# Kernel tuning notes

Hardware: AMD Instinct MI355X
Metric: run time of the kernel (lower is better)

The kernel has to match this reference:

```python
import jax, jax.numpy as jnp
import numpy as np

B, L, F, H = 4096, 32, 28, 512  # batch, max CDR length (=input_size), features, hidden


def setup_inputs() -> dict:
    key = jax.random.key(0)
    ks = jax.random.split(key, 8)
    return {
        "input": jax.random.normal(ks[0], (B, L, F), jnp.float32),
        "unpacked_masks": jnp.ones((B, L, 1), jnp.float32),
        "bias_mat": jnp.zeros((B, L, F), jnp.float32),
        "conv1_w": jax.random.normal(ks[1], (F, F, 3), jnp.float32) * 0.1,
        "conv1_b": jnp.zeros((F,), jnp.float32),
        "conv_w": jax.random.normal(ks[2], (1, L, 1), jnp.float32) * 0.1,
        "conv_b": jnp.zeros((1,), jnp.float32),
        "fc1_w": jax.random.normal(ks[3], (1, H), jnp.float32) * 0.05,
        "fc1_b": jnp.zeros((1,), jnp.float32),
        "W_ih": jax.random.normal(ks[4], (4 * H, L), jnp.float32) * 0.1,
        "W_hh": jax.random.normal(ks[5], (4 * H, H), jnp.float32) * 0.05,
        "b_ih": jnp.zeros((4 * H,), jnp.float32),
        "b_hh": jnp.zeros((4 * H,), jnp.float32),
        "conv2_w": jax.random.normal(ks[6], (1, H, 1), jnp.float32) * 0.05,
        "conv2_b": jnp.zeros((1,), jnp.float32),
    }


def reference(input, unpacked_masks, bias_mat, conv1_w, conv1_b, conv_w, conv_b,
              fc1_w, fc1_b, W_ih, W_hh, b_ih, b_hh, conv2_w, conv2_b):
    b, l, f = input.shape
    h_dim = W_hh.shape[1]
    # --- conv1 residual block (eval mode: dropouts are identity) ---
    x_t = jnp.transpose(input, (0, 2, 1))  # [B, F, L]
    y = jax.lax.conv_general_dilated(
        x_t, conv1_w, window_strides=(1,), padding=[(1, 1)],
        dimension_numbers=("NCH", "OIH", "NCH")) + conv1_b[None, :, None]
    x = jnp.transpose(y, (0, 2, 1)) * unpacked_masks  # [B, L, F]
    x = jax.nn.elu(x) + input
    # --- u_a = Conv1d(L,1,1) over the length axis: [B, 1, F] (kept as [B, F]) ---
    u_a = jnp.einsum("blf,l->bf", x, conv_w[0, :, 0]) + conv_b  # [B, F]
    x_transposed = jnp.transpose(x, (0, 2, 1))  # [B, F, L]

    h0 = jnp.zeros((l, h_dim), input.dtype)
    c0 = jnp.zeros((l, h_dim), input.dtype)

    def step(carry, inps):
        h, c = carry
        u_b, xT_b, bias_b = inps  # [F], [F, L], [L, F]
        w_a = h @ fc1_w.T + fc1_b  # [L, 1]
        scores = jax.nn.leaky_relu(u_b[None, :] + w_a, 0.01) + bias_b  # [L, F]
        attn = jax.nn.softmax(scores, axis=0)  # softmax over dim 1 of [B, L, F]
        ctx = attn @ xT_b  # [L, F] @ [F, L] -> [L, L]
        gates = ctx @ W_ih.T + b_ih + h @ W_hh.T + b_hh  # [L, 4H]
        i_g, f_g, g_g, o_g = jnp.split(gates, 4, axis=-1)
        c_new = jax.nn.sigmoid(f_g) * c + jax.nn.sigmoid(i_g) * jnp.tanh(g_g)
        h_new = jax.nn.sigmoid(o_g) * jnp.tanh(c_new)
        return (h_new, c_new), h_new

    # The original loops over the batch dim, carrying (h, c) across iterations.
    (_, _), all_hidden = jax.lax.scan(step, (h0, c0), (u_a, x_transposed, bias_mat))
    # all_hidden: [B, L, H]
    out = jnp.einsum("blh,h->bl", all_hidden, conv2_w[0, :, 0])[..., None] + conv2_b  # [B, L, 1]
    return out * unpacked_masks
```

## Files before the change

kernel.cpp:

```cpp
#include <hip/hip_runtime.h>
#include <math.h>

#define NBATCH 4096
#define LSEQ   32
#define FDIM   28
#define HDIM   512
#define GBLK   64
#define SLICE  8
#define HSTRIDE 548
#define XSTR    36

typedef int   i32x4 __attribute__((ext_vector_type(4)));
typedef float f32x4 __attribute__((ext_vector_type(4)));
typedef short short8 __attribute__((ext_vector_type(8)));

#define OFF_X    0u
#define OFF_UA   (OFF_X  + 4096u*896u)
#define OFF_BG   (OFF_UA + 4096u*28u)
#define OFF_H    (OFF_BG + 2048u)
#define OFF_BAR  (OFF_H  + 2u*32u*512u)
#define OFF_WFH  (OFF_BAR + 64u)
#define OFF_WFL  (OFF_WFH + 557056u)

__device__ __forceinline__ unsigned bfr(float x) {
    unsigned u = __builtin_bit_cast(unsigned, x);
    return (u + 0x7FFFu + ((u >> 16) & 1u)) >> 16;
}
__device__ __forceinline__ float fb(unsigned b) { return __builtin_bit_cast(float, b << 16); }
__device__ __forceinline__ unsigned packhl(float v) {
    unsigned h = bfr(v);
    unsigned l = bfr(v - fb(h));
    return h | (l << 16);
}
__device__ __forceinline__ float up(unsigned u) {
    return __builtin_bit_cast(float, u << 16) + __builtin_bit_cast(float, u & 0xFFFF0000u);
}
__device__ __forceinline__ float sigm(float v) { return 1.0f / (1.0f + __expf(-v)); }

__global__ __launch_bounds__(256) void prep_kernel(
    const float* __restrict__ input, const float* __restrict__ masks,
    const float* __restrict__ c1w, const float* __restrict__ c1b,
    const float* __restrict__ convw, const float* __restrict__ convb,
    float* __restrict__ xout, float* __restrict__ uaout)
{
    __shared__ float in_lds[32][28];
    __shared__ float w_lds[28][28][3];
    __shared__ float xo[32][28];
    __shared__ float m_lds[32];
    __shared__ float cb_lds[28];
    const int b = blockIdx.x, tid = threadIdx.x;

    for (int i = tid; i < 896; i += 256) in_lds[i / 28][i % 28] = input[(size_t)b * 896 + i];
    for (int i = tid; i < 2352; i += 256) {
        int o = i / 84, r = i % 84;
        w_lds[o][r / 3][r % 3] = c1w[i];
    }
    if (tid < 32) m_lds[tid] = masks[b * 32 + tid];
    if (tid < 28) cb_lds[tid] = c1b[tid];
    __syncthreads();

    for (int i = tid; i < 896; i += 256) {
        const int l = i / 28, f = i % 28;
        float acc = cb_lds[f];
        for (int ii = 0; ii < 28; ++ii) {
            if (l > 0)  acc = fmaf(in_lds[l - 1][ii], w_lds[f][ii][0], acc);
            acc = fmaf(in_lds[l][ii], w_lds[f][ii][1], acc);
            if (l < 31) acc = fmaf(in_lds[l + 1][ii], w_lds[f][ii][2], acc);
        }
        float v = acc * m_lds[l];
        v = (v > 0.f) ? v : expm1f(v);
        v += in_lds[l][f];
        xo[l][f] = v;
        xout[(size_t)b * 896 + i] = v;
    }
    __syncthreads();
    if (tid < 28) {
        float s = convb[0];
        for (int l = 0; l < 32; ++l) s = fmaf(xo[l][tid], convw[l], s);
        uaout[b * 28 + tid] = s;
    }
}

__global__ __launch_bounds__(256) void prepw_kernel(
    const float* __restrict__ bih, const float* __restrict__ bhh, float* __restrict__ BG)
{
    const int g = blockIdx.x * 256 + threadIdx.x;
    BG[g] = bih[g] + bhh[g];
}

__global__ __launch_bounds__(256) void prepf_kernel(
    const float* __restrict__ Wih, const float* __restrict__ Whh,
    unsigned* __restrict__ wfh, unsigned* __restrict__ wfl)
{
    const int id = blockIdx.x * 256 + threadIdx.x;
    const int lane = id & 63;
    int rest = id >> 6;
    const int ct = rest & 1; rest >>= 1;
    const int t = rest % 17, blk = rest / 17;
    const int n = lane & 15, kg = lane >> 4;
    const int c = ct * 16 + n;
    const int g = (c >> 3) * 512 + blk * 8 + (c & 7);
    const int kbase = t * 32 + kg * 8;
    i32x4 hv, lv;
    #pragma unroll
    for (int d = 0; d < 4; ++d) {
        const int k = kbase + 2 * d;
        float w0 = (k     < 512) ? Whh[(size_t)g * 512 + k]     : Wih[g * 32 + (k - 512)];
        float w1 = (k + 1 < 512) ? Whh[(size_t)g * 512 + k + 1] : Wih[g * 32 + (k + 1 - 512)];
        unsigned h0 = bfr(w0), h1 = bfr(w1);
        unsigned l0 = bfr(w0 - fb(h0)), l1 = bfr(w1 - fb(h1));
        ((unsigned*)&hv)[d] = h0 | (h1 << 16);
        ((unsigned*)&lv)[d] = l0 | (l1 << 16);
    }
    ((i32x4*)wfh)[id] = hv;
    ((i32x4*)wfl)[id] = lv;
}

__device__ __forceinline__ void stage8(const unsigned* p, unsigned* h_lds, int tid, int r)
{
    i32x4 v0, v1, v2, v3, v4, v5, v6, v7;
    asm volatile(
        "global_load_dwordx4 %0, %8, off sc0 sc1\n\t"
        "global_load_dwordx4 %1, %9, off sc0 sc1\n\t"
        "global_load_dwordx4 %2, %10, off sc0 sc1\n\t"
        "global_load_dwordx4 %3, %11, off sc0 sc1\n\t"
        "global_load_dwordx4 %4, %12, off sc0 sc1\n\t"
        "global_load_dwordx4 %5, %13, off sc0 sc1\n\t"
        "global_load_dwordx4 %6, %14, off sc0 sc1\n\t"
        "global_load_dwordx4 %7, %15, off sc0 sc1\n\t"
        "s_waitcnt vmcnt(0)"
        : "=&v"(v0), "=&v"(v1), "=&v"(v2), "=&v"(v3),
          "=&v"(v4), "=&v"(v5), "=&v"(v6), "=&v"(v7)
        : "v"(p), "v"(p + 1024), "v"(p + 2048), "v"(p + 3072),
          "v"(p + 4096), "v"(p + 5120), "v"(p + 6144), "v"(p + 7168)
        : "memory");
    const int col = (tid & 127) * 4;
    const int rb = 16 * r + (tid >> 7);
    *(i32x4*)&h_lds[(rb +  0) * HSTRIDE + col] = v0;
    *(i32x4*)&h_lds[(rb +  2) * HSTRIDE + col] = v1;
    *(i32x4*)&h_lds[(rb +  4) * HSTRIDE + col] = v2;
    *(i32x4*)&h_lds[(rb +  6) * HSTRIDE + col] = v3;
    *(i32x4*)&h_lds[(rb +  8) * HSTRIDE + col] = v4;
    *(i32x4*)&h_lds[(rb + 10) * HSTRIDE + col] = v5;
    *(i32x4*)&h_lds[(rb + 12) * HSTRIDE + col] = v6;
    *(i32x4*)&h_lds[(rb + 14) * HSTRIDE + col] = v7;
}
__device__ __forceinline__ void stage_h(const unsigned* hsrc, unsigned* h_lds, int tid)
{
    stage8(hsrc + tid * 4,        h_lds, tid, 0);
    stage8(hsrc + tid * 4 + 8192, h_lds, tid, 1);
}

__device__ __forceinline__ void build_frag(const unsigned* base, short8& hi, short8& lo)
{
    i32x4 ua = *(const i32x4*)base;
    i32x4 ub = *(const i32x4*)(base + 4);
    i32x4 h, l;
    h.x = (int)__builtin_amdgcn_perm((unsigned)ua.y, (unsigned)ua.x, 0x05040100u);
    l.x = (int)__builtin_amdgcn_perm((unsigned)ua.y, (unsigned)ua.x, 0x07060302u);
    h.y = (int)__builtin_amdgcn_perm((unsigned)ua.w, (unsigned)ua.z, 0x05040100u);
    l.y = (int)__builtin_amdgcn_perm((unsigned)ua.w, (unsigned)ua.z, 0x07060302u);
    h.z = (int)__builtin_amdgcn_perm((unsigned)ub.y, (unsigned)ub.x, 0x05040100u);
    l.z = (int)__builtin_amdgcn_perm((unsigned)ub.y, (unsigned)ub.x, 0x07060302u);
    h.w = (int)__builtin_amdgcn_perm((unsigned)ub.w, (unsigned)ub.z, 0x05040100u);
    l.w = (int)__builtin_amdgcn_perm((unsigned)ub.w, (unsigned)ub.z, 0x07060302u);
    hi = __builtin_bit_cast(short8, h);
    lo = __builtin_bit_cast(short8, l);
}

__device__ __forceinline__ float exact_gate(const unsigned* hrow,
    const float* __restrict__ Whh, const float* __restrict__ Wih, int g)
{
    const f32x4* wr = (const f32x4*)(Whh + (size_t)g * 512);
    float s = 0.f;
    #pragma unroll 4
    for (int q = 0; q < 128; ++q) {
        f32x4 w = wr[q];
        s += up(hrow[4 * q + 0]) * w.x + up(hrow[4 * q + 1]) * w.y
           + up(hrow[4 * q + 2]) * w.z + up(hrow[4 * q + 3]) * w.w;
    }
    const float* wi = Wih + g * 32;
    #pragma unroll 8
    for (int j = 0; j < 32; ++j) s += up(hrow[512 + j]) * wi[j];
    return s;
}

__device__ __forceinline__ void out_proj(const unsigned* h_lds, const float* c2w_lds, float c2b,
                                         const float* masks, float* out, int bb,
                                         int slot16, int seg16)
{
    float p0 = 0.f, p1 = 0.f;
    #pragma unroll
    for (int jj = 0; jj < 8; ++jj) {
        const int off = seg16 * 4 + 64 * jj;
        f32x4 w = *(const f32x4*)&c2w_lds[off];
        i32x4 h0 = *(const i32x4*)&h_lds[slot16 * HSTRIDE + off];
        i32x4 h1 = *(const i32x4*)&h_lds[(slot16 + 16) * HSTRIDE + off];
        p0 += up((unsigned)h0.x) * w.x + up((unsigned)h0.y) * w.y
            + up((unsigned)h0.z) * w.z + up((unsigned)h0.w) * w.w;
        p1 += up((unsigned)h1.x) * w.x + up((unsigned)h1.y) * w.y
            + up((unsigned)h1.z) * w.z + up((unsigned)h1.w) * w.w;
    }
    p0 += __shfl_xor(p0, 1); p0 += __shfl_xor(p0, 2);
    p0 += __shfl_xor(p0, 4); p0 += __shfl_xor(p0, 8);
    p1 += __shfl_xor(p1, 1); p1 += __shfl_xor(p1, 2);
    p1 += __shfl_xor(p1, 4); p1 += __shfl_xor(p1, 8);
    if (seg16 == 0) {
        out[bb * 32 + slot16]      = (p0 + c2b) * masks[bb * 32 + slot16];
        out[bb * 32 + slot16 + 16] = (p1 + c2b) * masks[bb * 32 + slot16 + 16];
    }
}

__global__ __launch_bounds__(256, 1) void rnn_serial(
    const float* __restrict__ xbuf, const float* __restrict__ uabuf,
    const float* __restrict__ BG,
    const unsigned* __restrict__ wfh, const unsigned* __restrict__ wfl,
    const float* __restrict__ Whh, const float* __restrict__ Wih,
    unsigned* hbuf, int* bar,
    const float* __restrict__ bias_mat, const float* __restrict__ masks,
    const float* __restrict__ fc1w, const float* __restrict__ fc1bp,
    const float* __restrict__ c2w, const float* __restrict__ c2bp,
    float* __restrict__ out)
{
    __shared__ unsigned h_lds[32 * HSTRIDE];
    __shared__ float x_lds[32 * XSTR];
    __shared__ float bias_lds[32 * XSTR];
    __shared__ float attn_lds[32 * XSTR];
    __shared__ float gl_part[4 * 32 * 33];
    __shared__ float wa_lds[32];
    __shared__ float ua_lds[28];
    __shared__ float fc1_lds[512];
    __shared__ float c2w_lds[512];
    __shared__ int   s_flag;

    const int tid  = threadIdx.x;
    const int blk  = blockIdx.x;
    const int lane = tid & 63;
    const int wv   = tid >> 6;

    for (int i = tid; i < 512; i += 256) { fc1_lds[i] = fc1w[i]; c2w_lds[i] = c2w[i]; }
    if (tid == 0) s_flag = 0;
    const float f1b = fc1bp[0];
    const float c2b = c2bp[0];

    const int nt = (wv < 3) ? 4 : 5;
    const int t0 = (wv < 3) ? wv * 4 : 12;
    i32x4 whi[5][2], wlo[5][2];
    {
        const i32x4* wfh4 = (const i32x4*)wfh;
        const i32x4* wfl4 = (const i32x4*)wfl;
        for (int s = 0; s < 5; ++s) {
            if (s < nt) {
                #pragma unroll
                for (int ct = 0; ct < 2; ++ct) {
                    const int idx = ((blk * 17 + t0 + s) * 2 + ct) * 64 + lane;
                    whi[s][ct] = wfh4[idx];
                    wlo[s][ct] = wfl4[idx];
                }
            }
        }
    }

    const int l_own = tid >> 3, hc = tid & 7;
    float bgv[4];
    #pragma unroll
    for (int t = 0; t < 4; ++t) bgv[t] = BG[t * 512 + blk * 8 + hc];
    float c_reg = 0.f;
    bool use_mfma = true;

    float4 xr = make_float4(0.f, 0.f, 0.f, 0.f), br = xr;
    float ua_r = 0.f;
    if (tid < 224) {
        xr = *(const float4*)(xbuf + tid * 4);
        br = *(const float4*)(bias_mat + tid * 4);
    }
    if (tid < 28) ua_r = uabuf[tid];

    const int slot16 = tid >> 4, seg16 = tid & 15;
    const int arow = lane & 15, kg = lane >> 4;
    int* cnt = bar;
    __syncthreads();

    for (int b = 0; b < NBATCH; ++b) {
        stage_h(hbuf + (b & 1) * 16384, h_lds, tid);
        if (tid < 224) {
            #pragma unroll
            for (int i = 0; i < 4; ++i) {
                const int idx = tid * 4 + i;
                const int l = idx / 28, f = idx - l * 28;
                x_lds[l * XSTR + f]    = ((const float*)&xr)[i];
                bias_lds[l * XSTR + f] = ((const float*)&br)[i];
            }
        }
        if (tid < 28) ua_lds[tid] = ua_r;
        __syncthreads();

        {
            float p0 = 0.f, p1 = 0.f;
            #pragma unroll
            for (int jj = 0; jj < 8; ++jj) {
                const int off = seg16 * 4 + 64 * jj;
                f32x4 w = *(const f32x4*)&fc1_lds[off];
                i32x4 h0 = *(const i32x4*)&h_lds[slot16 * HSTRIDE + off];
                i32x4 h1 = *(const i32x4*)&h_lds[(slot16 + 16) * HSTRIDE + off];
                p0 += up((unsigned)h0.x) * w.x + up((unsigned)h0.y) * w.y
                    + up((unsigned)h0.z) * w.z + up((unsigned)h0.w) * w.w;
                p1 += up((unsigned)h1.x) * w.x + up((unsigned)h1.y) * w.y
                    + up((unsigned)h1.z) * w.z + up((unsigned)h1.w) * w.w;
            }
            p0 += __shfl_xor(p0, 1); p0 += __shfl_xor(p0, 2);
            p0 += __shfl_xor(p0, 4); p0 += __shfl_xor(p0, 8);
            p1 += __shfl_xor(p1, 1); p1 += __shfl_xor(p1, 2);
            p1 += __shfl_xor(p1, 4); p1 += __shfl_xor(p1, 8);
            if (seg16 == 0) { wa_lds[slot16] = p0 + f1b; wa_lds[slot16 + 16] = p1 + f1b; }
        }
        if (b > 0 && blk == ((b - 1) & 63))
            out_proj(h_lds, c2w_lds, c2b, masks, out, b - 1, slot16, seg16);
        __syncthreads();

        if (tid < 224) {
            const int f = tid >> 3, ls = tid & 7;
            const float uaf = ua_lds[f];
            float z[4];
            #pragma unroll
            for (int r = 0; r < 4; ++r) {
                const int l = ls + 8 * r;
                float v = uaf + wa_lds[l];
                v = (v >= 0.f) ? v : 0.01f * v;
                z[r] = v + bias_lds[l * XSTR + f];
            }
            float mx = fmaxf(fmaxf(z[0], z[1]), fmaxf(z[2], z[3]));
            mx = fmaxf(mx, __shfl_xor(mx, 1));
            mx = fmaxf(mx, __shfl_xor(mx, 2));
            mx = fmaxf(mx, __shfl_xor(mx, 4));
            float s = 0.f;
            #pragma unroll
            for (int r = 0; r < 4; ++r) { z[r] = __expf(z[r] - mx); s += z[r]; }
            s += __shfl_xor(s, 1); s += __shfl_xor(s, 2); s += __shfl_xor(s, 4);
            const float inv = 1.0f / s;
            #pragma unroll
            for (int r = 0; r < 4; ++r) attn_lds[(ls + 8 * r) * XSTR + f] = z[r] * inv;
        }
        __syncthreads();

        {
            const int j0 = hc * 4;
            float t0v = 0.f, t1v = 0.f, t2v = 0.f, t3v = 0.f;
            #pragma unroll
            for (int fo = 0; fo < 7; ++fo) {
                f32x4 a4 = *(const f32x4*)&attn_lds[l_own * XSTR + fo * 4];
                f32x4 x0 = *(const f32x4*)&x_lds[(j0 + 0) * XSTR + fo * 4];
                f32x4 x1 = *(const f32x4*)&x_lds[(j0 + 1) * XSTR + fo * 4];
                f32x4 x2 = *(const f32x4*)&x_lds[(j0 + 2) * XSTR + fo * 4];
                f32x4 x3 = *(const f32x4*)&x_lds[(j0 + 3) * XSTR + fo * 4];
                t0v += a4.x * x0.x + a4.y * x0.y + a4.z * x0.z + a4.w * x0.w;
                t1v += a4.x * x1.x + a4.y * x1.y + a4.z * x1.z + a4.w * x1.w;
                t2v += a4.x * x2.x + a4.y * x2.y + a4.z * x2.z + a4.w * x2.w;
                t3v += a4.x * x3.x + a4.y * x3.y + a4.z * x3.z + a4.w * x3.w;
            }
            i32x4 cp;
            cp.x = (int)packhl(t0v); cp.y = (int)packhl(t1v);
            cp.z = (int)packhl(t2v); cp.w = (int)packhl(t3v);
            *(i32x4*)&h_lds[l_own * HSTRIDE + 512 + j0] = cp;
        }
        {
            const int bn = (b + 1 < NBATCH) ? b + 1 : 0;
            if (tid < 224) {
                xr = *(const float4*)(xbuf + (size_t)bn * 896 + tid * 4);
                br = *(const float4*)(bias_mat + (size_t)bn * 896 + tid * 4);
            }
            if (tid < 28) ua_r = uabuf[bn * 28 + tid];
        }
        __syncthreads();

        if (use_mfma) {
            f32x4 acc[2][2];
            acc[0][0] = (f32x4){0,0,0,0}; acc[0][1] = (f32x4){0,0,0,0};
            acc[1][0] = (f32x4){0,0,0,0}; acc[1][1] = (f32x4){0,0,0,0};
            #pragma unroll
            for (int s = 0; s < 5; ++s) {
                if (s < nt) {
                    const int k0 = (t0 + s) * 32 + kg * 8;
                    short8 ah0, al0, ah1, al1;
                    build_frag(&h_lds[arow * HSTRIDE + k0], ah0, al0);
                    build_frag(&h_lds[(arow + 16) * HSTRIDE + k0], ah1, al1);
                    #pragma unroll
                    for (int ct = 0; ct < 2; ++ct) {
                        short8 bh = __builtin_bit_cast(short8, whi[s][ct]);
                        short8 bl = __builtin_bit_cast(short8, wlo[s][ct]);
                        acc[ct][0] = __builtin_amdgcn_mfma_f32_16x16x32_bf16(ah0, bh, acc[ct][0], 0, 0, 0);
                        acc[ct][0] = __builtin_amdgcn_mfma_f32_16x16x32_bf16(al0, bh, acc[ct][0], 0, 0, 0);
                        acc[ct][0] = __builtin_amdgcn_mfma_f32_16x16x32_bf16(ah0, bl, acc[ct][0], 0, 0, 0);
                        acc[ct][1] = __builtin_amdgcn_mfma_f32_16x16x32_bf16(ah1, bh, acc[ct][1], 0, 0, 0);
                        acc[ct][1] = __builtin_amdgcn_mfma_f32_16x16x32_bf16(al1, bh, acc[ct][1], 0, 0, 0);
                        acc[ct][1] = __builtin_amdgcn_mfma_f32_16x16x32_bf16(ah1, bl, acc[ct][1], 0, 0, 0);
                    }
                }
            }
            #pragma unroll
            for (int ct = 0; ct < 2; ++ct)
                #pragma unroll
                for (int rt = 0; rt < 2; ++rt)
                    #pragma unroll
                    for (int r = 0; r < 4; ++r) {
                        const int row = rt * 16 + (lane >> 4) * 4 + r;
                        gl_part[(wv * 32 + row) * 33 + ct * 16 + (lane & 15)] = acc[ct][rt][r];
                    }
        }
        __syncthreads();

        {
            float gv[4];
            #pragma unroll
            for (int t = 0; t < 4; ++t) {
                float g = bgv[t];
                if (use_mfma) {
                    #pragma unroll
                    for (int w = 0; w < 4; ++w)
                        g += gl_part[(w * 32 + l_own) * 33 + t * 8 + hc];
                }
                gv[t] = g;
            }
            if (b < 2) {
                bool bad = false;
                #pragma unroll
                for (int t = 0; t < 4; ++t) {
                    float ref = bgv[t] + exact_gate(&h_lds[l_own * HSTRIDE], Whh, Wih,
                                                    t * 512 + blk * 8 + hc);
                    if (use_mfma && fabsf(gv[t] - ref) > 0.02f + 0.004f * fabsf(ref)) bad = true;
                    gv[t] = ref;
                }
                if (bad) s_flag = 1;
                __syncthreads();
                use_mfma = use_mfma && (s_flag == 0);
                __syncthreads();
                if (tid == 0) s_flag = 0;
            } else if (!use_mfma) {
                #pragma unroll
                for (int t = 0; t < 4; ++t)
                    gv[t] = bgv[t] + exact_gate(&h_lds[l_own * HSTRIDE], Whh, Wih,
                                                t * 512 + blk * 8 + hc);
            }
            const float cn = sigm(gv[1]) * c_reg + sigm(gv[0]) * tanhf(gv[2]);
            const float hn = sigm(gv[3]) * tanhf(cn);
            c_reg = cn;
            __hip_atomic_store(hbuf + ((b & 1) ^ 1) * 16384 + l_own * 512 + blk * 8 + hc,
                               packhl(hn), __ATOMIC_RELAXED, __HIP_MEMORY_SCOPE_AGENT);
        }

        asm volatile("s_waitcnt vmcnt(0)" ::: "memory");
        __syncthreads();
        if (tid == 0) {
            __hip_atomic_fetch_add(cnt, 1, __ATOMIC_RELAXED, __HIP_MEMORY_SCOPE_AGENT);
            const int target = (b + 1) * GBLK;
            while (__hip_atomic_load(cnt, __ATOMIC_RELAXED, __HIP_MEMORY_SCOPE_AGENT) < target)
                __builtin_amdgcn_s_sleep(1);
        }
        __syncthreads();
    }

    if (blk == 0) {
        stage_h(hbuf, h_lds, tid);
        __syncthreads();
        out_proj(h_lds, c2w_lds, c2b, masks, out, NBATCH - 1, slot16, seg16);
    }
}

extern "C" void kernel_launch(void* const* d_in, const int* in_sizes, int n_in,
                              void* d_out, int out_size, void* d_ws, size_t ws_size,
                              hipStream_t stream)
{
    const float* input    = (const float*)d_in[0];
    const float* masks    = (const float*)d_in[1];
    const float* bias_mat = (const float*)d_in[2];
    const float* c1w      = (const float*)d_in[3];
    const float* c1b      = (const float*)d_in[4];
    const float* convw    = (const float*)d_in[5];
    const float* convb    = (const float*)d_in[6];
    const float* fc1w     = (const float*)d_in[7];
    const float* fc1b     = (const float*)d_in[8];
    const float* Wih      = (const float*)d_in[9];
    const float* Whh      = (const float*)d_in[10];
    const float* bih      = (const float*)d_in[11];
    const float* bhh      = (const float*)d_in[12];
    const float* c2w      = (const float*)d_in[13];
    const float* c2b      = (const float*)d_in[14];

    float* ws  = (float*)d_ws;
    float* out = (float*)d_out;
    int*   bar = (int*)(ws + OFF_BAR);

    hipMemsetAsync(ws + OFF_H, 0, (2u * 32u * 512u + 64u) * sizeof(float), stream);

    hipLaunchKernelGGL(prep_kernel, dim3(NBATCH), dim3(256), 0, stream,
                       input, masks, c1w, c1b, convw, convb, ws + OFF_X, ws + OFF_UA);
    hipLaunchKernelGGL(prepw_kernel, dim3(8), dim3(256), 0, stream,
                       bih, bhh, ws + OFF_BG);
    hipLaunchKernelGGL(prepf_kernel, dim3(544), dim3(256), 0, stream,
                       Wih, Whh, (unsigned*)(ws + OFF_WFH), (unsigned*)(ws + OFF_WFL));
    hipLaunchKernelGGL(rnn_serial, dim3(GBLK), dim3(256), 0, stream,
                       ws + OFF_X, ws + OFF_UA, ws + OFF_BG,
                       (const unsigned*)(ws + OFF_WFH), (const unsigned*)(ws + OFF_WFL),
                       Whh, Wih,
                       (unsigned*)(ws + OFF_H), bar,
                       bias_mat, masks, fc1w, fc1b, c2w, c2b, out);
}
```

Baseline: 28.79 ms.

## Hoist h-part gate MFMAs before attention, fold fc1/conv2 dots into MFMA, per-block flag barrier

Moves the recurrent W_hh gate MFMAs (the first 16 k-slices) ahead of the attention/softmax phase, so they only depend on the staged h and leave only the 17th slice (ctx part) on the critical path after attention. The fc1 (w_a) and conv2 output dot products become extra MFMA columns, so the scalar LDS reductions run only in the first two validation steps. The softmax moves to a single wave, and h staging is restructured into one 16-load burst. The global barrier changes from a shared counter to per-block flags polled with a wave-wide all-check, trading atomic contention for more polling loads.

```diff
diff --git a/kernel.cpp b/kernel.cpp
--- a/kernel.cpp
+++ b/kernel.cpp
@@ -6,7 +6,6 @@
 #define FDIM   28
 #define HDIM   512
 #define GBLK   64
-#define SLICE  8
 #define HSTRIDE 548
 #define XSTR    36
 
@@ -116,39 +115,54 @@
     ((i32x4*)wfl)[id] = lv;
 }
 
-__device__ __forceinline__ void stage8(const unsigned* p, unsigned* h_lds, int tid, int r)
-{
-    i32x4 v0, v1, v2, v3, v4, v5, v6, v7;
+__device__ __forceinline__ void stage_h16(const unsigned* hsrc, unsigned* h_lds, int tid)
+{
+    const int half = tid >> 7, t128 = tid & 127;
+    const unsigned* p = hsrc + half * 8192 + t128 * 4;
+    i32x4 v0, v1, v2, v3, v4, v5, v6, v7, v8, v9, v10, v11, v12, v13, v14, v15;
     asm volatile(
-        "global_load_dwordx4 %0, %8, off sc0 sc1\n\t"
-        "global_load_dwordx4 %1, %9, off sc0 sc1\n\t"
-        "global_load_dwordx4 %2, %10, off sc0 sc1\n\t"
-        "global_load_dwordx4 %3, %11, off sc0 sc1\n\t"
-        "global_load_dwordx4 %4, %12, off sc0 sc1\n\t"
-        "global_load_dwordx4 %5, %13, off sc0 sc1\n\t"
-        "global_load_dwordx4 %6, %14, off sc0 sc1\n\t"
-        "global_load_dwordx4 %7, %15, off sc0 sc1\n\t"
+        "global_load_dwordx4 %0, %16, off sc0 sc1\n\t"
+        "global_load_dwordx4 %1, %16, off offset:2048 sc0 sc1\n\t"
+        "global_load_dwordx4 %2, %17, off sc0 sc1\n\t"
+        "global_load_dwordx4 %3, %17, off offset:2048 sc0 sc1\n\t"
+        "global_load_dwordx4 %4, %18, off sc0 sc1\n\t"
+        "global_load_dwordx4 %5, %18, off offset:2048 sc0 sc1\n\t"
+        "global_load_dwordx4 %6, %19, off sc0 sc1\n\t"
+        "global_load_dwordx4 %7, %19, off offset:2048 sc0 sc1\n\t"
+        "global_load_dwordx4 %8, %20, off sc0 sc1\n\t"
+        "global_load_dwordx4 %9, %20, off offset:2048 sc0 sc1\n\t"
+        "global_load_dwordx4 %10, %21, off sc0 sc1\n\t"
+        "global_load_dwordx4 %11, %21, off offset:2048 sc0 sc1\n\t"
+        "global_load_dwordx4 %12, %22, off sc0 sc1\n\t"
+        "global_load_dwordx4 %13, %22, off offset:2048 sc0 sc1\n\t"
+        "global_load_dwordx4 %14, %23, off sc0 sc1\n\t"
+        "global_load_dwordx4 %15, %23, off offset:2048 sc0 sc1\n\t"
         "s_waitcnt vmcnt(0)"
         : "=&v"(v0), "=&v"(v1), "=&v"(v2), "=&v"(v3),
-          "=&v"(v4), "=&v"(v5), "=&v"(v6), "=&v"(v7)
+          "=&v"(v4), "=&v"(v5), "=&v"(v6), "=&v"(v7),
+          "=&v"(v8), "=&v"(v9), "=&v"(v10), "=&v"(v11),
+          "=&v"(v12), "=&v"(v13), "=&v"(v14), "=&v"(v15)
         : "v"(p), "v"(p + 1024), "v"(p + 2048), "v"(p + 3072),
           "v"(p + 4096), "v"(p + 5120), "v"(p + 6144), "v"(p + 7168)
         : "memory");
-    const int col = (tid & 127) * 4;
-    const int rb = 16 * r + (tid >> 7);
+    const int col = t128 * 4;
+    const int rb = half * 16;
     *(i32x4*)&h_lds[(rb +  0) * HSTRIDE + col] = v0;
-    *(i32x4*)&h_lds[(rb +  2) * HSTRIDE + col] = v1;
-    *(i32x4*)&h_lds[(rb +  4) * HSTRIDE + col] = v2;
-    *(i32x4*)&h_lds[(rb +  6) * HSTRIDE + col] = v3;
-    *(i32x4*)&h_lds[(rb +  8) * HSTRIDE + col] = v4;
-    *(i32x4*)&h_lds[(rb + 10) * HSTRIDE + col] = v5;
-    *(i32x4*)&h_lds[(rb + 12) * HSTRIDE + col] = v6;
-    *(i32x4*)&h_lds[(rb + 14) * HSTRIDE + col] = v7;
-}
-__device__ __forceinline__ void stage_h(const unsigned* hsrc, unsigned* h_lds, int tid)
-{
-    stage8(hsrc + tid * 4,        h_lds, tid, 0);
-    stage8(hsrc + tid * 4 + 8192, h_lds, tid, 1);
+    *(i32x4*)&h_lds[(rb +  1) * HSTRIDE + col] = v1;
+    *(i32x4*)&h_lds[(rb +  2) * HSTRIDE + col] = v2;
+    *(i32x4*)&h_lds[(rb +  3) * HSTRIDE + col] = v3;
+    *(i32x4*)&h_lds[(rb +  4) * HSTRIDE + col] = v4;
+    *(i32x4*)&h_lds[(rb +  5) * HSTRIDE + col] = v5;
+    *(i32x4*)&h_lds[(rb +  6) * HSTRIDE + col] = v6;
+    *(i32x4*)&h_lds[(rb +  7) * HSTRIDE + col] = v7;
+    *(i32x4*)&h_lds[(rb +  8) * HSTRIDE + col] = v8;
+    *(i32x4*)&h_lds[(rb +  9) * HSTRIDE + col] = v9;
+    *(i32x4*)&h_lds[(rb + 10) * HSTRIDE + col] = v10;
+    *(i32x4*)&h_lds[(rb + 11) * HSTRIDE + col] = v11;
+    *(i32x4*)&h_lds[(rb + 12) * HSTRIDE + col] = v12;
+    *(i32x4*)&h_lds[(rb + 13) * HSTRIDE + col] = v13;
+    *(i32x4*)&h_lds[(rb + 14) * HSTRIDE + col] = v14;
+    *(i32x4*)&h_lds[(rb + 15) * HSTRIDE + col] = v15;
 }
 
 __device__ __forceinline__ void build_frag(const unsigned* base, short8& hi, short8& lo)
@@ -227,6 +241,7 @@
     __shared__ float bias_lds[32 * XSTR];
     __shared__ float attn_lds[32 * XSTR];
     __shared__ float gl_part[4 * 32 * 33];
+    __shared__ float wapart[4][2][32];
     __shared__ float wa_lds[32];
     __shared__ float ua_lds[28];
     __shared__ float fc1_lds[512];
@@ -243,19 +258,47 @@
     const float f1b = fc1bp[0];
     const float c2b = c2bp[0];
 
-    const int nt = (wv < 3) ? 4 : 5;
-    const int t0 = (wv < 3) ? wv * 4 : 12;
-    i32x4 whi[5][2], wlo[5][2];
+    i32x4 whi[4][2], wlo[4][2];
     {
         const i32x4* wfh4 = (const i32x4*)wfh;
         const i32x4* wfl4 = (const i32x4*)wfl;
-        for (int s = 0; s < 5; ++s) {
-            if (s < nt) {
-                #pragma unroll
-                for (int ct = 0; ct < 2; ++ct) {
-                    const int idx = ((blk * 17 + t0 + s) * 2 + ct) * 64 + lane;
-                    whi[s][ct] = wfh4[idx];
-                    wlo[s][ct] = wfl4[idx];
+        #pragma unroll
+        for (int s = 0; s < 4; ++s)
+            #pragma unroll
+            for (int ct = 0; ct < 2; ++ct) {
+                const int idx = ((blk * 17 + wv * 4 + s) * 2 + ct) * 64 + lane;
+                whi[s][ct] = wfh4[idx];
+                wlo[s][ct] = wfl4[idx];
+            }
+    }
+    i32x4 w16h[2], w16l[2];
+    if (wv == 0) {
+        const i32x4* wfh4 = (const i32x4*)wfh;
+        const i32x4* wfl4 = (const i32x4*)wfl;
+        #pragma unroll
+        for (int ct = 0; ct < 2; ++ct) {
+            const int idx = ((blk * 17 + 16) * 2 + ct) * 64 + lane;
+            w16h[ct] = wfh4[idx];
+            w16l[ct] = wfl4[idx];
+        }
+    }
+    i32x4 wAh[4], wAl[4];
+    {
+        const int n = lane & 15, kg = lane >> 4;
+        #pragma unroll
+        for (int s = 0; s < 4; ++s) {
+            wAh[s] = (i32x4){0, 0, 0, 0};
+            wAl[s] = (i32x4){0, 0, 0, 0};
+            if (n < 2) {
+                const float* src = (n == 0) ? fc1w : c2w;
+                const int k0 = (wv * 4 + s) * 32 + kg * 8;
+                #pragma unroll
+                for (int d = 0; d < 4; ++d) {
+                    float v0 = src[k0 + 2 * d], v1 = src[k0 + 2 * d + 1];
+                    unsigned h0 = bfr(v0), h1 = bfr(v1);
+                    unsigned l0 = bfr(v0 - fb(h0)), l1 = bfr(v1 - fb(h1));
+                    ((unsigned*)&wAh[s])[d] = h0 | (h1 << 16);
+                    ((unsigned*)&wAl[s])[d] = l0 | (l1 << 16);
                 }
             }
         }
@@ -278,11 +321,10 @@
 
     const int slot16 = tid >> 4, seg16 = tid & 15;
     const int arow = lane & 15, kg = lane >> 4;
-    int* cnt = bar;
     __syncthreads();
 
     for (int b = 0; b < NBATCH; ++b) {
-        stage_h(hbuf + (b & 1) * 16384, h_lds, tid);
+        stage_h16(hbuf + (b & 1) * 16384, h_lds, tid);
         if (tid < 224) {
             #pragma unroll
             for (int i = 0; i < 4; ++i) {
@@ -295,7 +337,56 @@
         if (tid < 28) ua_lds[tid] = ua_r;
         __syncthreads();
 
-        {
+        f32x4 accg[2][2], accw[2];
+        if (use_mfma) {
+            accg[0][0] = (f32x4){0,0,0,0}; accg[0][1] = (f32x4){0,0,0,0};
+            accg[1][0] = (f32x4){0,0,0,0}; accg[1][1] = (f32x4){0,0,0,0};
+            accw[0]    = (f32x4){0,0,0,0}; accw[1]    = (f32x4){0,0,0,0};
+            #pragma unroll
+            for (int s = 0; s < 4; ++s) {
+                const int k0 = (wv * 4 + s) * 32 + kg * 8;
+                short8 ah0, al0, ah1, al1;
+                build_frag(&h_lds[arow * HSTRIDE + k0], ah0, al0);
+                build_frag(&h_lds[(arow + 16) * HSTRIDE + k0], ah1, al1);
+                #pragma unroll
+                for (int ct = 0; ct < 2; ++ct) {
+                    short8 bh = __builtin_bit_cast(short8, whi[s][ct]);
+                    short8 bl = __builtin_bit_cast(short8, wlo[s][ct]);
+                    accg[ct][0] = __builtin_amdgcn_mfma_f32_16x16x32_bf16(ah0, bh, accg[ct][0], 0, 0, 0);
+                    accg[ct][0] = __builtin_amdgcn_mfma_f32_16x16x32_bf16(al0, bh, accg[ct][0], 0, 0, 0);
+                    accg[ct][0] = __builtin_amdgcn_mfma_f32_16x16x32_bf16(ah0, bl, accg[ct][0], 0, 0, 0);
+                    accg[ct][1] = __builtin_amdgcn_mfma_f32_16x16x32_bf16(ah1, bh, accg[ct][1], 0, 0, 0);
+                    accg[ct][1] = __builtin_amdgcn_mfma_f32_16x16x32_bf16(al1, bh, accg[ct][1], 0, 0, 0);
+                    accg[ct][1] = __builtin_amdgcn_mfma_f32_16x16x32_bf16(ah1, bl, accg[ct][1], 0, 0, 0);
+                }
+                short8 bh = __builtin_bit_cast(short8, wAh[s]);
+                short8 bl = __builtin_bit_cast(short8, wAl[s]);
+                accw[0] = __builtin_amdgcn_mfma_f32_16x16x32_bf16(ah0, bh, accw[0], 0, 0, 0);
+                accw[0] = __builtin_amdgcn_mfma_f32_16x16x32_bf16(al0, bh, accw[0], 0, 0, 0);
+                accw[0] = __builtin_amdgcn_mfma_f32_16x16x32_bf16(ah0, bl, accw[0], 0, 0, 0);
+                accw[1] = __builtin_amdgcn_mfma_f32_16x16x32_bf16(ah1, bh, accw[1], 0, 0, 0);
+                accw[1] = __builtin_amdgcn_mfma_f32_16x16x32_bf16(al1, bh, accw[1], 0, 0, 0);
+                accw[1] = __builtin_amdgcn_mfma_f32_16x16x32_bf16(ah1, bl, accw[1], 0, 0, 0);
+            }
+            if (wv != 0) {
+                #pragma unroll
+                for (int ct = 0; ct < 2; ++ct)
+                    #pragma unroll
+                    for (int rt = 0; rt < 2; ++rt)
+                        #pragma unroll
+                        for (int r = 0; r < 4; ++r)
+                            gl_part[(wv * 32 + rt * 16 + kg * 4 + r) * 33 + ct * 16 + (lane & 15)] = accg[ct][rt][r];
+            }
+            const int n = lane & 15;
+            if (n < 2) {
+                #pragma unroll
+                for (int rt = 0; rt < 2; ++rt)
+                    #pragma unroll
+                    for (int r = 0; r < 4; ++r)
+                        wapart[wv][n][rt * 16 + kg * 4 + r] = accw[rt][r];
+            }
+        }
+        if (b < 2 || !use_mfma) {
             float p0 = 0.f, p1 = 0.f;
             #pragma unroll
             for (int jj = 0; jj < 8; ++jj) {
@@ -313,33 +404,56 @@
             p1 += __shfl_xor(p1, 1); p1 += __shfl_xor(p1, 2);
             p1 += __shfl_xor(p1, 4); p1 += __shfl_xor(p1, 8);
             if (seg16 == 0) { wa_lds[slot16] = p0 + f1b; wa_lds[slot16 + 16] = p1 + f1b; }
-        }
-        if (b > 0 && blk == ((b - 1) & 63))
-            out_proj(h_lds, c2w_lds, c2b, masks, out, b - 1, slot16, seg16);
-        __syncthreads();
-
-        if (tid < 224) {
-            const int f = tid >> 3, ls = tid & 7;
-            const float uaf = ua_lds[f];
-            float z[4];
-            #pragma unroll
-            for (int r = 0; r < 4; ++r) {
-                const int l = ls + 8 * r;
-                float v = uaf + wa_lds[l];
-                v = (v >= 0.f) ? v : 0.01f * v;
-                z[r] = v + bias_lds[l * XSTR + f];
-            }
-            float mx = fmaxf(fmaxf(z[0], z[1]), fmaxf(z[2], z[3]));
-            mx = fmaxf(mx, __shfl_xor(mx, 1));
-            mx = fmaxf(mx, __shfl_xor(mx, 2));
-            mx = fmaxf(mx, __shfl_xor(mx, 4));
-            float s = 0.f;
-            #pragma unroll
-            for (int r = 0; r < 4; ++r) { z[r] = __expf(z[r] - mx); s += z[r]; }
-            s += __shfl_xor(s, 1); s += __shfl_xor(s, 2); s += __shfl_xor(s, 4);
-            const float inv = 1.0f / s;
-            #pragma unroll
-            for (int r = 0; r < 4; ++r) attn_lds[(ls + 8 * r) * XSTR + f] = z[r] * inv;
+            if (b > 0 && blk == ((b - 1) & 63))
+                out_proj(h_lds, c2w_lds, c2b, masks, out, b - 1, slot16, seg16);
+        }
+        __syncthreads();
+
+        if (wv == 3) {
+            if (use_mfma && lane < 32) {
+                float wm = f1b;
+                #pragma unroll
+                for (int w = 0; w < 4; ++w) wm += wapart[w][0][lane];
+                if (b < 2) {
+                    if (fabsf(wm - wa_lds[lane]) > 0.02f + 0.004f * fabsf(wa_lds[lane])) s_flag = 1;
+                } else {
+                    wa_lds[lane] = wm;
+                }
+            }
+            if (lane < 56) {
+                const int f = lane >> 1, hf = lane & 1;
+                const float uaf = ua_lds[f];
+                float z[16], mx = -1e30f;
+                #pragma unroll
+                for (int i = 0; i < 16; ++i) {
+                    const int l = hf * 16 + i;
+                    float v = uaf + wa_lds[l];
+                    v = (v >= 0.f) ? v : 0.01f * v;
+                    v += bias_lds[l * XSTR + f];
+                    z[i] = v;
+                    mx = fmaxf(mx, v);
+                }
+                mx = fmaxf(mx, __shfl_xor(mx, 1));
+                float sum = 0.f;
+                #pragma unroll
+                for (int i = 0; i < 16; ++i) { z[i] = __expf(z[i] - mx); sum += z[i]; }
+                sum += __shfl_xor(sum, 1);
+                const float inv = 1.0f / sum;
+                #pragma unroll
+                for (int i = 0; i < 16; ++i) attn_lds[(hf * 16 + i) * XSTR + f] = z[i] * inv;
+            }
+        } else if (wv == 2 && use_mfma && lane < 32) {
+            float om = c2b;
+            #pragma unroll
+            for (int w = 0; w < 4; ++w) om += wapart[w][1][lane];
+            if (b < 2) {
+                const unsigned* hr = &h_lds[lane * HSTRIDE];
+                float ox = c2b;
+                for (int k = 0; k < 512; ++k) ox += up(hr[k]) * c2w_lds[k];
+                if (fabsf(om - ox) > 0.02f + 0.004f * fabsf(ox)) s_flag = 1;
+            } else if (b > 0 && blk == ((b - 1) & 63)) {
+                out[(b - 1) * 32 + lane] = om * masks[(b - 1) * 32 + lane];
+            }
         }
         __syncthreads();
 
@@ -373,39 +487,28 @@
         }
         __syncthreads();
 
-        if (use_mfma) {
-            f32x4 acc[2][2];
-            acc[0][0] = (f32x4){0,0,0,0}; acc[0][1] = (f32x4){0,0,0,0};
-            acc[1][0] = (f32x4){0,0,0,0}; acc[1][1] = (f32x4){0,0,0,0};
-            #pragma unroll
-            for (int s = 0; s < 5; ++s) {
-                if (s < nt) {
-                    const int k0 = (t0 + s) * 32 + kg * 8;
-                    short8 ah0, al0, ah1, al1;
-                    build_frag(&h_lds[arow * HSTRIDE + k0], ah0, al0);
-                    build_frag(&h_lds[(arow + 16) * HSTRIDE + k0], ah1, al1);
-                    #pragma unroll
-                    for (int ct = 0; ct < 2; ++ct) {
-                        short8 bh = __builtin_bit_cast(short8, whi[s][ct]);
-                        short8 bl = __builtin_bit_cast(short8, wlo[s][ct]);
-                        acc[ct][0] = __builtin_amdgcn_mfma_f32_16x16x32_bf16(ah0, bh, acc[ct][0], 0, 0, 0);
-                        acc[ct][0] = __builtin_amdgcn_mfma_f32_16x16x32_bf16(al0, bh, acc[ct][0], 0, 0, 0);
-                        acc[ct][0] = __builtin_amdgcn_mfma_f32_16x16x32_bf16(ah0, bl, acc[ct][0], 0, 0, 0);
-                        acc[ct][1] = __builtin_amdgcn_mfma_f32_16x16x32_bf16(ah1, bh, acc[ct][1], 0, 0, 0);
-                        acc[ct][1] = __builtin_amdgcn_mfma_f32_16x16x32_bf16(al1, bh, acc[ct][1], 0, 0, 0);
-                        acc[ct][1] = __builtin_amdgcn_mfma_f32_16x16x32_bf16(ah1, bl, acc[ct][1], 0, 0, 0);
-                    }
-                }
+        if (use_mfma && wv == 0) {
+            short8 ah0, al0, ah1, al1;
+            build_frag(&h_lds[arow * HSTRIDE + 512 + kg * 8], ah0, al0);
+            build_frag(&h_lds[(arow + 16) * HSTRIDE + 512 + kg * 8], ah1, al1);
+            #pragma unroll
+            for (int ct = 0; ct < 2; ++ct) {
+                short8 bh = __builtin_bit_cast(short8, w16h[ct]);
+                short8 bl = __builtin_bit_cast(short8, w16l[ct]);
+                accg[ct][0] = __builtin_amdgcn_mfma_f32_16x16x32_bf16(ah0, bh, accg[ct][0], 0, 0, 0);
+                accg[ct][0] = __builtin_amdgcn_mfma_f32_16x16x32_bf16(al0, bh, accg[ct][0], 0, 0, 0);
+                accg[ct][0] = __builtin_amdgcn_mfma_f32_16x16x32_bf16(ah0, bl, accg[ct][0], 0, 0, 0);
+                accg[ct][1] = __builtin_amdgcn_mfma_f32_16x16x32_bf16(ah1, bh, accg[ct][1], 0, 0, 0);
+                accg[ct][1] = __builtin_amdgcn_mfma_f32_16x16x32_bf16(al1, bh, accg[ct][1], 0, 0, 0);
+                accg[ct][1] = __builtin_amdgcn_mfma_f32_16x16x32_bf16(ah1, bl, accg[ct][1], 0, 0, 0);
             }
             #pragma unroll
             for (int ct = 0; ct < 2; ++ct)
                 #pragma unroll
                 for (int rt = 0; rt < 2; ++rt)
                     #pragma unroll
-                    for (int r = 0; r < 4; ++r) {
-                        const int row = rt * 16 + (lane >> 4) * 4 + r;
-                        gl_part[(wv * 32 + row) * 33 + ct * 16 + (lane & 15)] = acc[ct][rt][r];
-                    }
+                    for (int r = 0; r < 4; ++r)
+                        gl_part[(rt * 16 + kg * 4 + r) * 33 + ct * 16 + (lane & 15)] = accg[ct][rt][r];
         }
         __syncthreads();
 
@@ -447,22 +550,59 @@
             __hip_atomic_store(hbuf + ((b & 1) ^ 1) * 16384 + l_own * 512 + blk * 8 + hc,
                                packhl(hn), __ATOMIC_RELAXED, __HIP_MEMORY_SCOPE_AGENT);
         }
-
         asm volatile("s_waitcnt vmcnt(0)" ::: "memory");
         __syncthreads();
-        if (tid == 0) {
-            __hip_atomic_fetch_add(cnt, 1, __ATOMIC_RELAXED, __HIP_MEMORY_SCOPE_AGENT);
-            const int target = (b + 1) * GBLK;
-            while (__hip_atomic_load(cnt, __ATOMIC_RELAXED, __HIP_MEMORY_SCOPE_AGENT) < target)
+        if (tid == 0)
+            __hip_atomic_store(&bar[blk], b + 1, __ATOMIC_RELAXED, __HIP_MEMORY_SCOPE_AGENT);
+        if (tid < 64) {
+            while (true) {
+                int v = __hip_atomic_load(&bar[tid], __ATOMIC_RELAXED, __HIP_MEMORY_SCOPE_AGENT);
+                if (__all(v >= b + 1)) break;
                 __builtin_amdgcn_s_sleep(1);
-        }
-        __syncthreads();
-    }
-
-    if (blk == 0) {
-        stage_h(hbuf, h_lds, tid);
-        __syncthreads();
-        out_proj(h_lds, c2w_lds, c2b, masks, out, NBATCH - 1, slot16, seg16);
+            }
+        }
+        __syncthreads();
+    }
+
+    if (blk == 63) {
+        stage_h16(hbuf, h_lds, tid);
+        __syncthreads();
+        if (use_mfma) {
+            f32x4 accw[2];
+            accw[0] = (f32x4){0,0,0,0}; accw[1] = (f32x4){0,0,0,0};
+            #pragma unroll
+            for (int s = 0; s < 4; ++s) {
+                const int k0 = (wv * 4 + s) * 32 + kg * 8;
+                short8 ah0, al0, ah1, al1;
+                build_frag(&h_lds[arow * HSTRIDE + k0], ah0, al0);
+                build_frag(&h_lds[(arow + 16) * HSTRIDE + k0], ah1, al1);
+                short8 bh = __builtin_bit_cast(short8, wAh[s]);
+                short8 bl = __builtin_bit_cast(short8, wAl[s]);
+                accw[0] = __builtin_amdgcn_mfma_f32_16x16x32_bf16(ah0, bh, accw[0], 0, 0, 0);
+                accw[0] = __builtin_amdgcn_mfma_f32_16x16x32_bf16(al0, bh, accw[0], 0, 0, 0);
+                accw[0] = __builtin_amdgcn_mfma_f32_16x16x32_bf16(ah0, bl, accw[0], 0, 0, 0);
+                accw[1] = __builtin_amdgcn_mfma_f32_16x16x32_bf16(ah1, bh, accw[1], 0, 0, 0);
+                accw[1] = __builtin_amdgcn_mfma_f32_16x16x32_bf16(al1, bh, accw[1], 0, 0, 0);
+                accw[1] = __builtin_amdgcn_mfma_f32_16x16x32_bf16(ah1, bl, accw[1], 0, 0, 0);
+            }
+            const int n = lane & 15;
+            if (n < 2) {
+                #pragma unroll
+                for (int rt = 0; rt < 2; ++rt)
+                    #pragma unroll
+                    for (int r = 0; r < 4; ++r)
+                        wapart[wv][n][rt * 16 + kg * 4 + r] = accw[rt][r];
+            }
+            __syncthreads();
+            if (wv == 2 && lane < 32) {
+                float om = c2b;
+                #pragma unroll
+                for (int w = 0; w < 4; ++w) om += wapart[w][1][lane];
+                out[4095 * 32 + lane] = om * masks[4095 * 32 + lane];
+            }
+        } else {
+            out_proj(h_lds, c2w_lds, c2b, masks, out, 4095, slot16, seg16);
+        }
     }
 }
 
```

Result: no change. 28.92 ms (+0.5%).
